# Performance work log

Hardware: AMD Instinct MI355X
Metric: run time of the kernel (lower is better)

## Reference

```python
import jax, jax.numpy as jnp
import numpy as np
from jax import lax

STRIDES = [8, 16, 32, 64, 128]
NUM_CLASSES = 80
PRE_NMS_THRESH = 0.05
PRE_NMS_TOP_N = 1000
NMS_THRESH = 0.6
MAX_DET = 100
IMG_SIZE = 800.0
BBOX_W = (10.0, 10.0, 5.0, 5.0)
SCALE_CLAMP = float(np.log(1000.0 / 16.0))  # Box2BoxTransform clamp


def conv3x3(x, w, b):
    y = lax.conv_general_dilated(x, w, (1, 1), 'SAME',
                                 dimension_numbers=('NCHW', 'OIHW', 'NCHW'))
    return y + b[None, :, None, None]


def conv1x1(x, w, b):
    return jnp.einsum('nchw,kc->nkhw', x, w) + b[None, :, None, None]


def make_anchors(H, W, stride):
    # one square anchor per location, size = 8 * stride (ATSS), offset 0.5
    size = 8.0 * stride
    xs = (jnp.arange(W, dtype=jnp.float32) + 0.5) * stride
    ys = (jnp.arange(H, dtype=jnp.float32) + 0.5) * stride
    cy, cx = jnp.meshgrid(ys, xs, indexing='ij')
    half = size / 2.0
    return jnp.stack([cx - half, cy - half, cx + half, cy + half], -1).reshape(-1, 4)


def decode(deltas, anchors):
    # Box2BoxTransform.apply_deltas with weights (10,10,5,5)
    wx, wy, ww, wh = BBOX_W
    aw = anchors[..., 2] - anchors[..., 0]
    ah = anchors[..., 3] - anchors[..., 1]
    acx = anchors[..., 0] + 0.5 * aw
    acy = anchors[..., 1] + 0.5 * ah
    dx = deltas[..., 0] / wx
    dy = deltas[..., 1] / wy
    dw = jnp.minimum(deltas[..., 2] / ww, SCALE_CLAMP)
    dh = jnp.minimum(deltas[..., 3] / wh, SCALE_CLAMP)
    pcx = dx * aw + acx
    pcy = dy * ah + acy
    pw = jnp.exp(dw) * aw
    ph = jnp.exp(dh) * ah
    boxes = jnp.stack([pcx - 0.5 * pw, pcy - 0.5 * ph,
                       pcx + 0.5 * pw, pcy + 0.5 * ph], -1)
    return jnp.clip(boxes, 0.0, IMG_SIZE)


def iou_one_vs_all(box, boxes):
    x1 = jnp.maximum(box[0], boxes[:, 0])
    y1 = jnp.maximum(box[1], boxes[:, 1])
    x2 = jnp.minimum(box[2], boxes[:, 2])
    y2 = jnp.minimum(box[3], boxes[:, 3])
    inter = jnp.clip(x2 - x1, 0.0) * jnp.clip(y2 - y1, 0.0)
    a1 = (box[2] - box[0]) * (box[3] - box[1])
    a2 = (boxes[:, 2] - boxes[:, 0]) * (boxes[:, 3] - boxes[:, 1])
    return inter / (a1 + a2 - inter + 1e-9)


def nms_single(boxes, scores, classes):
    # class-aware greedy NMS via per-class coordinate offset (ml_nms trick)
    off = classes.astype(boxes.dtype)[:, None] * (2.0 * IMG_SIZE)
    ob = boxes + off

    def step(s, _):
        i = jnp.argmax(s)
        best = s[i]
        iou = iou_one_vs_all(ob[i], ob)
        s = jnp.where(iou > NMS_THRESH, -1.0, s)
        s = s.at[i].set(-1.0)
        return s, (i, best)

    _, (idx, kept) = lax.scan(step, scores, None, length=MAX_DET)
    valid = kept > 0
    out_boxes = jnp.where(valid[:, None], boxes[idx], 0.0)
    out_scores = jnp.where(valid, kept, 0.0)
    out_classes = jnp.where(valid, classes[idx], -1)
    return out_boxes, out_scores, out_classes


def atss_forward(feats, cls_tw, cls_tb, bbox_tw, bbox_tb,
                 wcls, bcls, wbox, bbox_b, wctr, bctr, scales):
    all_boxes, all_scores, all_classes = [], [], []
    for l, x in enumerate(feats):
        c = x
        b = x
        for i in range(cls_tw.shape[0]):  # 4 tower convs
            c = jax.nn.relu(conv3x3(c, cls_tw[i], cls_tb[i]))
            b = jax.nn.relu(conv3x3(b, bbox_tw[i], bbox_tb[i]))
        logits = conv1x1(c, wcls, bcls)               # [N,C,H,W]
        deltas = scales[l] * conv1x1(b, wbox, bbox_b)  # [N,4,H,W]
        ctr = conv1x1(b, wctr, bctr)                   # [N,1,H,W]
        N, C, H, W = logits.shape
        logits = logits.transpose(0, 2, 3, 1).reshape(N, H * W, C)
        deltas = deltas.transpose(0, 2, 3, 1).reshape(N, H * W, 4)
        ctr = ctr.transpose(0, 2, 3, 1).reshape(N, H * W)
        anchors = make_anchors(H, W, STRIDES[l])       # [HW,4]
        # ATSS inference scoring: sigmoid(cls) * sigmoid(centerness)
        s = jax.nn.sigmoid(logits) * jax.nn.sigmoid(ctr)[..., None]
        s = jnp.where(s > PRE_NMS_THRESH, s, 0.0)
        flat = s.reshape(N, -1)                        # [N, HW*C]
        k = min(PRE_NMS_TOP_N, flat.shape[1])
        vals, idx = lax.top_k(flat, k)
        aidx = idx // C
        cidx = idx % C
        d = jnp.take_along_axis(deltas, aidx[:, :, None], axis=1)  # [N,k,4]
        boxes = decode(d, anchors[aidx])
        # final score = sqrt(cls*ctr); safe sqrt to avoid inf grad at 0
        sc = jnp.sqrt(jnp.where(vals > 0, vals, 1.0)) * (vals > 0)
        all_boxes.append(boxes)
        all_scores.append(sc)
        all_classes.append(cidx)
    boxes = jnp.concatenate(all_boxes, 1)
    scores = jnp.concatenate(all_scores, 1)
    classes = jnp.concatenate(all_classes, 1)
    return jax.vmap(nms_single)(boxes, scores, classes)


def setup_inputs() -> dict:
    key = jax.random.key(0)
    ks = jax.random.split(key, 12)
    feats_hw = [(100, 100), (50, 50), (25, 25), (13, 13), (7, 7)]
    N, CIN, CH = 4, 256, 256
    inp = {}
    for i, (h, w) in enumerate(feats_hw):
        inp['p%d' % (i + 3)] = jax.random.normal(ks[i], (N, CIN, h, w), jnp.float32)
    inp['cls_tw'] = jax.random.normal(ks[5], (4, CH, CIN, 3, 3), jnp.float32) * 0.02
    inp['cls_tb'] = jnp.zeros((4, CH), jnp.float32)
    inp['bbox_tw'] = jax.random.normal(ks[6], (4, CH, CIN, 3, 3), jnp.float32) * 0.02
    inp['bbox_tb'] = jnp.zeros((4, CH), jnp.float32)
    inp['wcls'] = jax.random.normal(ks[7], (NUM_CLASSES, CH), jnp.float32) * 0.05
    inp['bcls'] = jnp.zeros((NUM_CLASSES,), jnp.float32)
    inp['wbox'] = jax.random.normal(ks[8], (4, CH), jnp.float32) * 0.05
    inp['bbox_b'] = jnp.zeros((4,), jnp.float32)
    inp['wctr'] = jax.random.normal(ks[9], (1, CH), jnp.float32) * 0.05
    inp['bctr'] = jnp.zeros((1,), jnp.float32)
    inp['scales'] = jnp.ones((5,), jnp.float32)
    return inp


def reference(p3, p4, p5, p6, p7, cls_tw, cls_tb, bbox_tw, bbox_tb,
              wcls, bcls, wbox, bbox_b, wctr, bctr, scales):
    feats = [p3, p4, p5, p6, p7]
    boxes, scores, classes = atss_forward(feats, cls_tw, cls_tb, bbox_tw, bbox_tb,
                                          wcls, bcls, wbox, bbox_b, wctr, bctr, scales)
    return boxes, scores, classes
```

## Files before the change

### kernel.cpp

```cpp
#include <hip/hip_runtime.h>
#include <math.h>

typedef short s8v __attribute__((ext_vector_type(8)));
typedef short s4v __attribute__((ext_vector_type(4)));
typedef float f4v __attribute__((ext_vector_type(4)));
typedef _Float16 h8v __attribute__((ext_vector_type(8)));

__device__ __forceinline__ float sigf(float x) { return 1.f / (1.f + expf(-x)); }
__device__ __forceinline__ float f16f(short v) {
  return (float)__builtin_bit_cast(_Float16, v);
}

#define SCALE_CLAMP 4.135166556742356f
#define IMG_SIZE 800.f
#define PLANE 14482432ull
#define W_SCALE 1024.f
#define A_SCALE 64.f
#define ACC_RESCALE 1.52587890625e-5f

__device__ __forceinline__ void split2(float x, short& h, short& l) {
  _Float16 hf = (_Float16)x;
  _Float16 lf = (_Float16)(x - (float)hf);
  h = __builtin_bit_cast(short, hf);
  l = __builtin_bit_cast(short, lf);
}

struct Geo {
  int tp[6];
  int TXa[5];
  int Ha[5], Wa[5], PWa[5], PHWa[5];
  int phwOff[5];
  int hwOff[5];
  int pb[6];
  int bb[6];
};

__global__ __launch_bounds__(256) void wtrans_k(const float* __restrict__ cls_tw,
                                                const float* __restrict__ bbox_tw,
                                                short* __restrict__ wt)
{
  const int total = 589824;
  for (int u = blockIdx.x * 256 + threadIdx.x; u < total; u += gridDim.x * 256) {
    int layer = u / 73728;
    int r = u - layer * 73728;
    int tap = r / 8192;  r -= tap * 8192;
    int cc  = r / 1024;  r -= cc * 1024;
    int qq  = r / 256;   int ko = r - qq * 256;
    int cibase = cc * 32 + qq * 8;
    const float* src = (layer < 4) ? (cls_tw + (size_t)layer * 589824)
                                   : (bbox_tw + (size_t)(layer - 4) * 589824);
    s8v hv, lv;
#pragma unroll
    for (int e = 0; e < 8; ++e) {
      float x = src[(size_t)ko * 2304 + (size_t)(cibase + e) * 9 + tap] * W_SCALE;
      short h, l; split2(x, h, l);
      hv[e] = h; lv[e] = l;
    }
    size_t dbase = (size_t)layer * 1179648 + (((size_t)tap * 8 + cc) * 4 + qq) * 2048 + (size_t)ko * 8;
    *(s8v*)(wt + dbase) = hv;
    *(s8v*)(wt + dbase + 589824) = lv;
  }
}

__global__ __launch_bounds__(256) void prep_all_k(const float* __restrict__ p3, const float* __restrict__ p4,
                                                  const float* __restrict__ p5, const float* __restrict__ p6,
                                                  const float* __restrict__ p7,
                                                  short* __restrict__ out, Geo g)
{
  __shared__ float tl[64][260];
  int bx = blockIdx.x, t = threadIdx.x, n = blockIdx.y;
  int l = 0; while (l < 4 && bx >= g.pb[l + 1]) ++l;
  const float* in = (l == 0) ? p3 : (l == 1) ? p4 : (l == 2) ? p5 : (l == 3) ? p6 : p7;
  int H = g.Ha[l], W = g.Wa[l], PW = g.PWa[l], PHW = g.PHWa[l], HW = H * W;
  int P0 = (bx - g.pb[l]) * 64;
  const float* inN = in + (size_t)n * HW * 256;
  int sub = t >> 6, pl = t & 63;
  int pos = P0 + pl;
  for (int i = 0; i < 64; ++i) {
    int ci = i * 4 + sub;
    tl[pl][ci] = (pos < HW) ? inN[(size_t)ci * HW + pos] : 0.f;
  }
  __syncthreads();
  int pl2 = t >> 2, cq = (t & 3) * 64;
  int pos2 = P0 + pl2;
  if (pos2 < HW) {
    int y = pos2 / W, x = pos2 - y * W;
    size_t oo = ((size_t)g.phwOff[l] * 4 + (size_t)n * PHW + (size_t)(y + 1) * PW + (x + 1)) * 256 + cq;
#pragma unroll
    for (int grp = 0; grp < 8; ++grp) {
      s8v hv, lv;
#pragma unroll
      for (int e = 0; e < 8; ++e) {
        short h, lo; split2(tl[pl2][cq + grp * 8 + e] * A_SCALE, h, lo);
        hv[e] = h; lv[e] = lo;
      }
      *(s8v*)(out + oo + grp * 8) = hv;
      *(s8v*)(out + PLANE + oo + grp * 8) = lv;
    }
  }
}

#define QS    112
#define QVALID 108
#define PSTR  3584
#define BSTR  7168
__global__ __launch_bounds__(256, 4) void conv_all_k(const short* __restrict__ in0,
                                                     const short* __restrict__ in1,
                                                     const short* __restrict__ wt0,
                                                     const short* __restrict__ wt1,
                                                     const float* __restrict__ bias0,
                                                     const float* __restrict__ bias1,
                                                     short* __restrict__ out0,
                                                     short* __restrict__ out1, Geo g)
{
  __shared__ short act_s[2 * BSTR];

  const int t = threadIdx.x;
  const int lane = t & 63, wave = t >> 6;
  const int wcol = wave & 1, wko = wave >> 1;
  const int tower = blockIdx.z >> 2;
  const int n = blockIdx.z & 3;
  const short* in   = tower ? in1 : in0;
  const short* wtL  = tower ? wt1 : wt0;
  const float* bias = tower ? bias1 : bias0;
  short* out        = tower ? out1 : out0;
  const int ko0 = blockIdx.y * 128;
  int bx = blockIdx.x;
  int l = 0; while (l < 4 && bx >= g.tp[l + 1]) ++l;
  const int H = g.Ha[l], W = g.Wa[l], PW = g.PWa[l], PHW = g.PHWa[l];
  const int lt = bx - g.tp[l];
  const int TX = g.TXa[l];
  const int ty = lt / TX, tx = lt - ty * TX;
  const int R0 = ty * 4, C0 = tx * 16;
  const size_t bi = ((size_t)g.phwOff[l] * 4 + (size_t)n * PHW) * 256;
  const short* inN = in + bi;
  short* outN = out + bi;

  const int r = lane & 15, q = lane >> 4;
  const int cb = wcol * 8;
  const short* wlane = wtL + (size_t)q * 2048 + (size_t)(ko0 + wko * 64 + r) * 8;

  int soff[2];
#pragma unroll
  for (int k = 0; k < 2; ++k) {
    int j = t + k * 256; if (j > 447) j = 447;
    int qq = j / QS, ppos = j - qq * QS;
    int lpos = ppos - 2 * qq; if (lpos < 0) lpos += QS;
    if (lpos >= QVALID) lpos = QVALID - 1;
    int row = lpos / 18, col = lpos - row * 18;
    int prow = R0 + row; if (prow > H + 1) prow = H + 1;
    int pcol = C0 + col; if (pcol > W + 1) pcol = W + 1;
    soff[k] = (prow * PW + pcol) * 256 + qq * 8;
  }

  f4v acc[2][4];
#pragma unroll
  for (int mi = 0; mi < 2; ++mi)
#pragma unroll
    for (int ni = 0; ni < 4; ++ni) { f4v z = {0.f, 0.f, 0.f, 0.f}; acc[mi][ni] = z; }

  auto stage = [&](int cc, int buf) {
#pragma unroll
    for (int k = 0; k < 2; ++k) {
      int j = t + k * 256;
      if (j < 448) {
#pragma unroll
        for (int p = 0; p < 2; ++p) {
          const short* src = inN + (size_t)p * PLANE + (size_t)(soff[k] + cc * 32);
          short* dst = &act_s[(size_t)buf * BSTR + (size_t)p * PSTR + (size_t)j * 8];
#if __has_builtin(__builtin_amdgcn_global_load_lds)
          __builtin_amdgcn_global_load_lds((const __attribute__((address_space(1))) void*)src,
                                           (__attribute__((address_space(3))) void*)dst, 16, 0, 0);
#else
          *(s8v*)dst = *(const s8v*)src;
#endif
        }
      }
    }
  };

  auto loadW = [&](s8v (&w)[2][2], int cc2, int tap2, int half) {
    const short* base = wlane + (size_t)(tap2 * 8 + cc2) * 8192 + half * 256;
#pragma unroll
    for (int p = 0; p < 2; ++p)
#pragma unroll
      for (int k = 0; k < 2; ++k)
        w[p][k] = *(const s8v*)(base + (size_t)p * 589824 + k * 128);
  };

  auto loadA = [&](s8v (&af)[2][2], int dy, int dx, int buf) {
    const int sbase = buf * BSTR;
#pragma unroll
    for (int mi = 0; mi < 2; ++mi) {
      int lp = (2 * mi + (r >> 3) + dy) * 18 + (cb + (r & 7) + dx) + 2 * q;
      if (lp >= QS) lp -= QS;
      int sl = q * QS + lp;
      af[0][mi] = *(const s8v*)&act_s[sbase + sl * 8];
      af[1][mi] = *(const s8v*)&act_s[sbase + PSTR + sl * 8];
    }
  };

  auto runHalf = [&](const s8v (&w)[2][2], const s8v (&af)[2][2], int half) {
    const int PA[3] = {0, 0, 1};
    const int PB[3] = {0, 1, 0};
    __builtin_amdgcn_s_setprio(1);
#pragma unroll
    for (int pp = 0; pp < 3; ++pp)
#pragma unroll
      for (int mi = 0; mi < 2; ++mi)
#pragma unroll
        for (int k = 0; k < 2; ++k)
          acc[mi][half * 2 + k] = __builtin_amdgcn_mfma_f32_16x16x32_f16(
              __builtin_bit_cast(h8v, af[PA[pp]][mi]),
              __builtin_bit_cast(h8v, w[PB[pp]][k]),
              acc[mi][half * 2 + k], 0, 0, 0);
    __builtin_amdgcn_s_setprio(0);
  };

  s8v wH0[2][2], wH1[2][2], afr[2][2];
  stage(0, 0);
  loadW(wH0, 0, 0, 0);
  __syncthreads();

  int cur = 0;
  for (int cc = 0; cc < 8; ++cc) {
    if (cc < 7) stage(cc + 1, cur ^ 1);
#pragma unroll
    for (int tap = 0; tap < 9; ++tap) {
      const int dy = tap / 3, dx = tap - dy * 3;
      loadW(wH1, cc, tap, 1);
      loadA(afr, dy, dx, cur);
      runHalf(wH0, afr, 0);
      int ntap = tap + 1, ncc = cc;
      if (ntap == 9) { ntap = 0; ++ncc; }
      if (ncc < 8) loadW(wH0, ncc, ntap, 0);
      runHalf(wH1, afr, 1);
    }
    __syncthreads();
    cur ^= 1;
  }

#pragma unroll
  for (int mi = 0; mi < 2; ++mi) {
#pragma unroll
    for (int ni = 0; ni < 4; ++ni) {
      int ko = ko0 + wko * 64 + ni * 16 + r;
      float bv = bias[ko];
#pragma unroll
      for (int reg = 0; reg < 4; ++reg) {
        int rm = q * 4 + reg;
        int orow = R0 + 2 * mi + (rm >> 3);
        int ocol = C0 + cb + (rm & 7);
        if (orow < H && ocol < W) {
          float real = acc[mi][ni][reg] * ACC_RESCALE + bv;
          float vv = fmaxf(real, 0.f) * A_SCALE;
          short h, lo; split2(vv, h, lo);
          size_t oo = ((size_t)(orow + 1) * PW + (ocol + 1)) * 256 + ko;
          outN[oo] = h; outN[PLANE + oo] = lo;
        }
      }
    }
  }
}

__global__ __launch_bounds__(256) void cls_head_k(const short* __restrict__ act,
                                                  const float* __restrict__ wcls,
                                                  const float* __restrict__ bcls,
                                                  float* __restrict__ score, Geo g)
{
  __shared__ int   p2s[64];
  __shared__ float as_[64][69];
  __shared__ float ws_[64][84];
  const int t = threadIdx.x;
  const int n = blockIdx.y;
  int bx = blockIdx.x;
  int l = 0; while (l < 4 && bx >= g.pb[l + 1]) ++l;
  const int H = g.Ha[l], W = g.Wa[l], PW = g.PWa[l], PHW = g.PHWa[l], HW = H * W;
  const int P0 = (bx - g.pb[l]) * 64;
  if (t < 64) {
    int p = P0 + t; if (p >= HW) p = HW - 1;
    int y = p / W, x = p - y * W;
    p2s[t] = (y + 1) * PW + x + 1;
  }
  __syncthreads();
  float accv[4][5];
#pragma unroll
  for (int i = 0; i < 4; ++i)
#pragma unroll
    for (int j = 0; j < 5; ++j) accv[i][j] = 0.f;

  const short* actN = act + ((size_t)g.phwOff[l] * 4 + (size_t)n * PHW) * 256;
  const int pg = t >> 4, cg = t & 15;
  const float inv = 1.f / A_SCALE;

  for (int c0 = 0; c0 < 256; c0 += 64) {
    for (int i = t; i < 1024; i += 256) {
      int pos = i >> 4, c4 = i & 15;
      size_t o = (size_t)p2s[pos] * 256 + c0 + c4 * 4;
      s4v hv = *(const s4v*)(actN + o);
      s4v lv = *(const s4v*)(actN + PLANE + o);
      float* dst = &as_[pos][c4 * 4];
#pragma unroll
      for (int e = 0; e < 4; ++e) dst[e] = (f16f(hv[e]) + f16f(lv[e])) * inv;
    }
    for (int i = t; i < 1280; i += 256) {
      int c = i >> 4, c4 = i & 15;
      float4 v = *(const float4*)(wcls + (size_t)c * 256 + c0 + c4 * 4);
      ws_[c4 * 4 + 0][c] = v.x; ws_[c4 * 4 + 1][c] = v.y;
      ws_[c4 * 4 + 2][c] = v.z; ws_[c4 * 4 + 3][c] = v.w;
    }
    __syncthreads();
#pragma unroll 8
    for (int ci = 0; ci < 64; ++ci) {
#pragma unroll
      for (int i = 0; i < 4; ++i) {
        float a = as_[pg * 4 + i][ci];
#pragma unroll
        for (int j = 0; j < 5; ++j)
          accv[i][j] = fmaf(a, ws_[ci][cg * 5 + j], accv[i][j]);
      }
    }
    __syncthreads();
  }
  float* sB = score + ((size_t)g.hwOff[l] * 4 + (size_t)n * HW) * 80;
#pragma unroll
  for (int i = 0; i < 4; ++i) {
    int p = P0 + pg * 4 + i;
    if (p >= HW) continue;
#pragma unroll
    for (int j = 0; j < 5; ++j) {
      int c = cg * 5 + j;
      sB[(size_t)p * 80 + c] = sigf(accv[i][j] + bcls[c]);
    }
  }
}

__global__ __launch_bounds__(256) void box_head_k(const short* __restrict__ act,
                                                  const float* __restrict__ wbox,
                                                  const float* __restrict__ bb,
                                                  const float* __restrict__ wctr,
                                                  const float* __restrict__ bc,
                                                  const float* __restrict__ scales,
                                                  float* __restrict__ score,
                                                  float* __restrict__ deltas, Geo g)
{
  int n = blockIdx.y;
  int bx = blockIdx.x;
  int l = 0; while (l < 4 && bx >= g.bb[l + 1]) ++l;
  const int H = g.Ha[l], W = g.Wa[l], PW = g.PWa[l], PHW = g.PHWa[l], HW = H * W;
  int p = (bx - g.bb[l]) * 256 + threadIdx.x;
  if (p >= HW) return;
  int y = p / W, x = p - y * W;
  const short* a = act + ((size_t)g.phwOff[l] * 4 + (size_t)n * PHW + (size_t)(y + 1) * PW + x + 1) * 256;
  const float inv = 1.f / A_SCALE;
  float d0 = 0, d1 = 0, d2 = 0, d3 = 0, ct = 0;
  for (int gI = 0; gI < 32; ++gI) {
    s8v hv = *(const s8v*)(a + gI * 8);
    s8v lv = *(const s8v*)(a + PLANE + gI * 8);
#pragma unroll
    for (int e = 0; e < 8; ++e) {
      float av = (f16f(hv[e]) + f16f(lv[e])) * inv;
      int c = gI * 8 + e;
      d0 = fmaf(av, wbox[c], d0);
      d1 = fmaf(av, wbox[256 + c], d1);
      d2 = fmaf(av, wbox[512 + c], d2);
      d3 = fmaf(av, wbox[768 + c], d3);
      ct = fmaf(av, wctr[c], ct);
    }
  }
  float sl = scales[l];
  float* dd = deltas + ((size_t)g.hwOff[l] * 4 + (size_t)n * HW + p) * 4;
  dd[0] = sl * (d0 + bb[0]); dd[1] = sl * (d1 + bb[1]);
  dd[2] = sl * (d2 + bb[2]); dd[3] = sl * (d3 + bb[3]);
  float sct = sigf(ct + bc[0]);
  float* sp = score + ((size_t)g.hwOff[l] * 4 + (size_t)n * HW + p) * 80;
#pragma unroll
  for (int i = 0; i < 20; ++i) {
    float4 v = ((float4*)sp)[i];
    v.x *= sct; v.y *= sct; v.z *= sct; v.w *= sct;
    v.x = (v.x > 0.05f) ? v.x : 0.f;
    v.y = (v.y > 0.05f) ? v.y : 0.f;
    v.z = (v.z > 0.05f) ? v.z : 0.f;
    v.w = (v.w > 0.05f) ? v.w : 0.f;
    ((float4*)sp)[i] = v;
  }
}

__global__ __launch_bounds__(256) void hist_k(const float* __restrict__ score,
                                              const unsigned* __restrict__ thr,
                                              unsigned* __restrict__ hist, int phase, Geo g)
{
  const int grp = blockIdx.y;
  const int l = grp >> 2, n = grp & 3;
  const int HW = g.Ha[l] * g.Wa[l];
  const int M = HW * 80;
  const float* s = score + ((size_t)g.hwOff[l] * 4 + (size_t)n * HW) * 80;
  unsigned* h = hist + grp * 2048;
  const unsigned* tr = thr + grp * 8;
  __shared__ unsigned lh[2048];
  for (int i = threadIdx.x; i < 2048; i += 256) lh[i] = 0u;
  __syncthreads();
  unsigned B1 = 0, pref = 0;
  if (phase == 1) B1 = tr[0];
  if (phase == 2) pref = (tr[0] << 11) | tr[1];
  for (int idx = blockIdx.x * 256 + threadIdx.x; idx < M; idx += gridDim.x * 256) {
    float v = s[idx];
    if (v > 0.f) {
      unsigned b = __float_as_uint(v);
      if (phase == 0) atomicAdd(&lh[b >> 20], 1u);
      else if (phase == 1) { if ((b >> 20) == B1) atomicAdd(&lh[(b >> 9) & 0x7FFu], 1u); }
      else { if ((b >> 9) == pref) atomicAdd(&lh[b & 0x1FFu], 1u); }
    }
  }
  __syncthreads();
  for (int i = threadIdx.x; i < 2048; i += 256) { unsigned v = lh[i]; if (v) atomicAdd(&h[i], v); }
}

__global__ __launch_bounds__(256) void scan_k(unsigned* __restrict__ hist,
                                              unsigned* __restrict__ thr, int phase)
{
  const int grp = blockIdx.x, t = threadIdx.x;
  unsigned* h  = hist + grp * 2048;
  unsigned* tr = thr + grp * 8;
  const int nb = (phase == 2) ? 512 : 2048;
  const int PB = nb / 256;
  unsigned target = 1000u;
  bool dead = false;
  if (phase >= 1) {
    target = 1000u - tr[2];
    if (tr[0] == 0xFFFFFFFFu) dead = true;
    if (phase == 2 && tr[1] == 0xFFFFFFFFu) dead = true;
  }
  __shared__ unsigned ps[256];
  __shared__ unsigned s_tot;
  const int hi = nb - t * PB;
  unsigned lsum = 0;
  for (int k = 0; k < PB; ++k) lsum += h[hi - 1 - k];
  ps[t] = lsum;
  __syncthreads();
  if (t == 0) {
    unsigned cum = 0;
    for (int i = 0; i < 256; ++i) { unsigned tmp = ps[i]; ps[i] = cum; cum += tmp; }
    s_tot = cum;
  }
  __syncthreads();
  unsigned exc = ps[t], tot = s_tot;
  if (!dead && tot >= target) {
    if (exc < target && exc + lsum >= target) {
      unsigned cum = exc; int bf = 0; unsigned above = 0;
      for (int k = 0; k < PB; ++k) {
        int bidx = hi - 1 - k;
        unsigned c = h[bidx];
        if (cum < target && cum + c >= target) { bf = bidx; above = cum; }
        cum += c;
      }
      if (phase == 0)      { tr[0] = (unsigned)bf; tr[2] = above; }
      else if (phase == 1) { tr[1] = (unsigned)bf; tr[2] = tr[2] + above; }
      else {
        unsigned T = (tr[0] << 20) | (tr[1] << 9) | (unsigned)bf;
        tr[3] = T; tr[4] = target - above;
      }
    }
  } else if (t == 0) {
    if (phase == 0)      { tr[0] = 0xFFFFFFFFu; tr[2] = 0u; }
    else if (phase == 1) { tr[1] = 0xFFFFFFFFu; }
    else                 { tr[3] = 0u; tr[4] = 0u; }
  }
  if (phase == 2 && t == 0) { tr[5] = 0u; tr[6] = 0u; }
}

__global__ __launch_bounds__(256) void select_k(const float* __restrict__ score,
                                                const float* __restrict__ deltas,
                                                unsigned* __restrict__ thr,
                                                float* __restrict__ cbox, float* __restrict__ csc,
                                                float* __restrict__ ccls, float* __restrict__ cgid,
                                                Geo g)
{
  const int grp = blockIdx.y;
  const int l = grp >> 2, n = grp & 3;
  const int W = g.Wa[l];
  const int HW = g.Ha[l] * W;
  const int M = HW * 80;
  const float stride_ = (float)(8 << l);
  const float* s = score + ((size_t)g.hwOff[l] * 4 + (size_t)n * HW) * 80;
  const float* dBase = deltas + ((size_t)g.hwOff[l] * 4 + (size_t)n * HW) * 4;
  unsigned* tr = thr + grp * 8;
  const unsigned T = tr[3], need = tr[4];
  for (int idx = blockIdx.x * 256 + threadIdx.x; idx < M; idx += gridDim.x * 256) {
    float v = s[idx];
    if (!(v > 0.f)) continue;
    unsigned b = __float_as_uint(v);
    int slot = -1;
    if (b > T) slot = (int)atomicAdd(&tr[5], 1u);
    else if (b == T) {
      unsigned e = atomicAdd(&tr[6], 1u);
      if (e < need) slot = (int)(1000u - need + e);
    }
    if (slot < 0) continue;
    int p = idx / 80, c = idx - p * 80;
    int y = p / W, x = p - y * W;
    const float* d = dBase + (size_t)p * 4;
    float sz  = 8.f * stride_;
    float acx = ((float)x + 0.5f) * stride_;
    float acy = ((float)y + 0.5f) * stride_;
    float dx = d[0] / 10.f, dy = d[1] / 10.f;
    float dw = fminf(d[2] / 5.f, SCALE_CLAMP);
    float dh = fminf(d[3] / 5.f, SCALE_CLAMP);
    float pcx = dx * sz + acx;
    float pcy = dy * sz + acy;
    float pw = expf(dw) * sz;
    float ph = expf(dh) * sz;
    float x1 = pcx - 0.5f * pw, y1_ = pcy - 0.5f * ph;
    float x2 = pcx + 0.5f * pw, y2_ = pcy + 0.5f * ph;
    x1  = fminf(fmaxf(x1, 0.f),  IMG_SIZE);
    y1_ = fminf(fmaxf(y1_, 0.f), IMG_SIZE);
    x2  = fminf(fmaxf(x2, 0.f),  IMG_SIZE);
    y2_ = fminf(fmaxf(y2_, 0.f), IMG_SIZE);
    int cslot = n * 5000 + l * 1000 + slot;
    ((float4*)cbox)[cslot] = make_float4(x1, y1_, x2, y2_);
    csc[cslot]  = sqrtf(v);
    ccls[cslot] = (float)c;
    cgid[cslot] = (float)(((unsigned)l << 20) | (unsigned)idx);
  }
}

__global__ __launch_bounds__(256) void nms_k(const float* __restrict__ cbox,
                                             const float* __restrict__ csc,
                                             const float* __restrict__ ccls,
                                             const float* __restrict__ cgid,
                                             float* __restrict__ outp)
{
  const int n = blockIdx.x, t = threadIdx.x;
  float sc[20], cl[20], gid[20], bx[20][4];
#pragma unroll
  for (int j = 0; j < 20; ++j) {
    int gidx = j * 256 + t;
    if (gidx < 5000) {
      sc[j] = csc[n * 5000 + gidx];
      float4 b = ((const float4*)cbox)[n * 5000 + gidx];
      bx[j][0] = b.x; bx[j][1] = b.y; bx[j][2] = b.z; bx[j][3] = b.w;
      cl[j]  = ccls[n * 5000 + gidx];
      gid[j] = cgid[n * 5000 + gidx];
    } else { sc[j] = -2.f; bx[j][0] = bx[j][1] = bx[j][2] = bx[j][3] = 0.f; cl[j] = 0.f; gid[j] = 1e9f; }
  }
  __shared__ float rv[4]; __shared__ int rg[4]; __shared__ float rgid[4];
  __shared__ float sbox[4]; __shared__ float scls; __shared__ float sval; __shared__ int sgi;

  for (int it = 0; it < 100; ++it) {
    float bv = -3.f; int bg = 0; float bgid = 2e9f;
#pragma unroll
    for (int j = 0; j < 20; ++j) {
      bool better = (sc[j] > bv) || (sc[j] == bv && gid[j] < bgid);
      if (better) { bv = sc[j]; bg = j * 256 + t; bgid = gid[j]; }
    }
    for (int off = 32; off; off >>= 1) {
      float ov = __shfl_xor(bv, off);
      int   og = __shfl_xor(bg, off);
      float oi = __shfl_xor(bgid, off);
      bool better = (ov > bv) || (ov == bv && oi < bgid);
      if (better) { bv = ov; bg = og; bgid = oi; }
    }
    int wid = t >> 6;
    if ((t & 63) == 0) { rv[wid] = bv; rg[wid] = bg; rgid[wid] = bgid; }
    __syncthreads();
    if (t == 0) {
      float fv = rv[0]; int fg = rg[0]; float fi = rgid[0];
      for (int w = 1; w < 4; ++w) {
        bool better = (rv[w] > fv) || (rv[w] == fv && rgid[w] < fi);
        if (better) { fv = rv[w]; fg = rg[w]; fi = rgid[w]; }
      }
      sval = fv; sgi = fg;
    }
    __syncthreads();
    float best_v = sval; int best_g = sgi;
    if (t == (best_g & 255)) {
      int j = best_g >> 8;
      sbox[0] = bx[j][0]; sbox[1] = bx[j][1]; sbox[2] = bx[j][2]; sbox[3] = bx[j][3];
      scls = cl[j];
    }
    __syncthreads();
    bool valid = best_v > 0.f;
    if (t == 0) {
      int base = n * 100 + it;
      outp[base * 4 + 0] = valid ? sbox[0] : 0.f;
      outp[base * 4 + 1] = valid ? sbox[1] : 0.f;
      outp[base * 4 + 2] = valid ? sbox[2] : 0.f;
      outp[base * 4 + 3] = valid ? sbox[3] : 0.f;
      outp[1600 + base] = valid ? best_v : 0.f;
      outp[2000 + base] = valid ? scls : -1.f;
    }
    float off_ = scls * (2.f * IMG_SIZE);
    float e0 = sbox[0] + off_, e1 = sbox[1] + off_, e2 = sbox[2] + off_, e3 = sbox[3] + off_;
    float a1 = (e2 - e0) * (e3 - e1);
#pragma unroll
    for (int j = 0; j < 20; ++j) {
      float o_ = cl[j] * (2.f * IMG_SIZE);
      float f0 = bx[j][0] + o_, f1 = bx[j][1] + o_, f2 = bx[j][2] + o_, f3 = bx[j][3] + o_;
      float xx1 = fmaxf(e0, f0), yy1 = fmaxf(e1, f1);
      float xx2 = fminf(e2, f2), yy2 = fminf(e3, f3);
      float inter = fmaxf(xx2 - xx1, 0.f) * fmaxf(yy2 - yy1, 0.f);
      float a2 = (f2 - f0) * (f3 - f1);
      float iou = inter / (a1 + a2 - inter + 1e-9f);
      if (iou > 0.6f) sc[j] = -1.f;
      if ((j * 256 + t) == best_g) sc[j] = -1.f;
    }
    __syncthreads();
  }
}

extern "C" void kernel_launch(void* const* d_in, const int* in_sizes, int n_in,
                              void* d_out, int out_size, void* d_ws, size_t ws_size,
                              hipStream_t stream)
{
  (void)in_sizes; (void)n_in; (void)out_size; (void)ws_size;
  const float* p3 = (const float*)d_in[0];
  const float* p4 = (const float*)d_in[1];
  const float* p5 = (const float*)d_in[2];
  const float* p6 = (const float*)d_in[3];
  const float* p7 = (const float*)d_in[4];
  const float* cls_tw  = (const float*)d_in[5];
  const float* cls_tb  = (const float*)d_in[6];
  const float* bbox_tw = (const float*)d_in[7];
  const float* bbox_tb = (const float*)d_in[8];
  const float* wcls    = (const float*)d_in[9];
  const float* bcls    = (const float*)d_in[10];
  const float* wbox    = (const float*)d_in[11];
  const float* bbox_b  = (const float*)d_in[12];
  const float* wctr    = (const float*)d_in[13];
  const float* bctr    = (const float*)d_in[14];
  const float* scales  = (const float*)d_in[15];
  float* out = (float*)d_out;

  Geo G;
  const int Hs[5] = {100, 50, 25, 13, 7};
  {
    int tpre = 0, ppre = 0, bpre = 0, phw = 0, hw = 0;
    for (int l = 0; l < 5; ++l) {
      int H = Hs[l], W = Hs[l];
      G.Ha[l] = H; G.Wa[l] = W; G.PWa[l] = W + 2; G.PHWa[l] = (H + 2) * (W + 2);
      G.TXa[l] = (W + 15) / 16;
      int TY = (H + 3) / 4;
      G.tp[l] = tpre;  tpre += G.TXa[l] * TY;
      G.pb[l] = ppre;  ppre += (H * W + 63) / 64;
      G.bb[l] = bpre;  bpre += (H * W + 255) / 256;
      G.phwOff[l] = phw; phw += G.PHWa[l];
      G.hwOff[l]  = hw;  hw  += H * W;
    }
    G.tp[5] = tpre; G.pb[5] = ppre; G.bb[5] = bpre;
  }
  const int nTiles = G.tp[5];
  const int nPrep  = G.pb[5];
  const int nBoxB  = G.bb[5];
  const int sumHW = 13343;
  const size_t scoreBytes  = (size_t)sumHW * 4 * 80 * 4;
  const size_t deltasBytes = (size_t)sumHW * 4 * 4 * 4;

  char* ws = (char*)d_ws;
  size_t off = 0;
  auto alloc = [&](size_t bytes) -> void* {
    off = (off + 255) & ~(size_t)255;
    void* p = ws + off; off += bytes; return p;
  };
  const size_t bufBytes = 2ull * PLANE * 2;

  short* wt     = (short*)alloc((size_t)8 * 2 * 589824 * 2);
  float* cbox   = (float*)alloc(4ull * 5000 * 4 * 4);
  float* csc    = (float*)alloc(4ull * 5000 * 4);
  float* ccls   = (float*)alloc(4ull * 5000 * 4);
  float* cgid   = (float*)alloc(4ull * 5000 * 4);
  unsigned* hist = (unsigned*)alloc(20ull * 2048 * 4);
  unsigned* thr  = (unsigned*)alloc(20ull * 8 * 4);
  short* A = (short*)alloc(bufBytes);
  short* B = (short*)alloc(bufBytes);
  float* score  = (float*)alloc(scoreBytes);
  float* deltas = (float*)alloc(deltasBytes);

  hipMemsetAsync(cbox, 0, 4ull * 5000 * 4 * 4, stream);
  hipMemsetAsync(csc,  0, 4ull * 5000 * 4, stream);
  hipMemsetAsync(ccls, 0, 4ull * 5000 * 4, stream);
  hipMemsetAsync(cgid, 0, 4ull * 5000 * 4, stream);
  hipMemsetAsync(thr,  0, 20ull * 8 * 4, stream);
  hipMemsetAsync(A, 0, bufBytes, stream);
  hipMemsetAsync(B, 0, bufBytes, stream);

  wtrans_k<<<1024, 256, 0, stream>>>(cls_tw, bbox_tw, wt);

  const size_t LSTRIDE = 2ull * 589824;
  dim3 cg(nTiles, 2, 4);

  prep_all_k<<<dim3(nPrep, 4), 256, 0, stream>>>(p3, p4, p5, p6, p7, A, G);
  conv_all_k<<<cg, 256, 0, stream>>>(A, A, wt + 0 * LSTRIDE, wt + 0 * LSTRIDE,
                                     cls_tb + 0 * 256, cls_tb + 0 * 256, B, B, G);
  conv_all_k<<<cg, 256, 0, stream>>>(B, B, wt + 1 * LSTRIDE, wt + 1 * LSTRIDE,
                                     cls_tb + 1 * 256, cls_tb + 1 * 256, A, A, G);
  conv_all_k<<<cg, 256, 0, stream>>>(A, A, wt + 2 * LSTRIDE, wt + 2 * LSTRIDE,
                                     cls_tb + 2 * 256, cls_tb + 2 * 256, B, B, G);
  conv_all_k<<<cg, 256, 0, stream>>>(B, B, wt + 3 * LSTRIDE, wt + 3 * LSTRIDE,
                                     cls_tb + 3 * 256, cls_tb + 3 * 256, A, A, G);
  cls_head_k<<<dim3(nPrep, 4), 256, 0, stream>>>(A, wcls, bcls, score, G);
  prep_all_k<<<dim3(nPrep, 4), 256, 0, stream>>>(p3, p4, p5, p6, p7, B, G);
  conv_all_k<<<cg, 256, 0, stream>>>(B, B, wt + 4 * LSTRIDE, wt + 4 * LSTRIDE,
                                     bbox_tb + 0 * 256, bbox_tb + 0 * 256, A, A, G);
  conv_all_k<<<cg, 256, 0, stream>>>(A, A, wt + 5 * LSTRIDE, wt + 5 * LSTRIDE,
                                     bbox_tb + 1 * 256, bbox_tb + 1 * 256, B, B, G);
  conv_all_k<<<cg, 256, 0, stream>>>(B, B, wt + 6 * LSTRIDE, wt + 6 * LSTRIDE,
                                     bbox_tb + 2 * 256, bbox_tb + 2 * 256, A, A, G);
  conv_all_k<<<cg, 256, 0, stream>>>(A, A, wt + 7 * LSTRIDE, wt + 7 * LSTRIDE,
                                     bbox_tb + 3 * 256, bbox_tb + 3 * 256, B, B, G);
  box_head_k<<<dim3(nBoxB, 4), 256, 0, stream>>>(B, wbox, bbox_b, wctr, bctr, scales,
                                                 score, deltas, G);

  const int hb = 196;
  for (int phase = 0; phase < 3; ++phase) {
    hipMemsetAsync(hist, 0, 20ull * 2048 * 4, stream);
    hist_k<<<dim3(hb, 20), 256, 0, stream>>>(score, thr, hist, phase, G);
    scan_k<<<20, 256, 0, stream>>>(hist, thr, phase);
  }
  select_k<<<dim3(hb, 20), 256, 0, stream>>>(score, deltas, thr, cbox, csc, ccls, cgid, G);

  nms_k<<<4, 256, 0, stream>>>(cbox, csc, ccls, cgid, out);
}
```

Before: 2.223 ms.

## Split NMS into per-class bucketed NMS blocks plus top-k merge

Replaces the single-block-per-image greedy NMS with three kernels. The first buckets candidates by class with packed score/id keys, the second runs independent per-class NMS in parallel blocks, and the third merges the per-class kept lists into the top 100. This exploits the fact that class-aware NMS only suppresses within a class, which removes the long serial 100-iteration loop over all 5000 candidates per image. The cost is two extra kernel launches and workspace buffers. The bucketing also uses shared-memory atomics, so ties may be ordered differently.

```diff
diff --git a/kernel.cpp b/kernel.cpp
--- a/kernel.cpp
+++ b/kernel.cpp
@@ -524,85 +524,140 @@
   }
 }
 
-__global__ __launch_bounds__(256) void nms_k(const float* __restrict__ cbox,
-                                             const float* __restrict__ csc,
-                                             const float* __restrict__ ccls,
-                                             const float* __restrict__ cgid,
-                                             float* __restrict__ outp)
-{
+__global__ __launch_bounds__(256) void nms_bucket_k(const float* __restrict__ cbox,
+                                                    const float* __restrict__ csc,
+                                                    const float* __restrict__ ccls,
+                                                    const float* __restrict__ cgid,
+                                                    float4* __restrict__ bbox2,
+                                                    unsigned long long* __restrict__ bkey2,
+                                                    int* __restrict__ coff)
+{
+  __shared__ unsigned cnt[80];
+  __shared__ unsigned off_s[81];
   const int n = blockIdx.x, t = threadIdx.x;
-  float sc[20], cl[20], gid[20], bx[20][4];
-#pragma unroll
-  for (int j = 0; j < 20; ++j) {
-    int gidx = j * 256 + t;
-    if (gidx < 5000) {
-      sc[j] = csc[n * 5000 + gidx];
-      float4 b = ((const float4*)cbox)[n * 5000 + gidx];
-      bx[j][0] = b.x; bx[j][1] = b.y; bx[j][2] = b.z; bx[j][3] = b.w;
-      cl[j]  = ccls[n * 5000 + gidx];
-      gid[j] = cgid[n * 5000 + gidx];
-    } else { sc[j] = -2.f; bx[j][0] = bx[j][1] = bx[j][2] = bx[j][3] = 0.f; cl[j] = 0.f; gid[j] = 1e9f; }
-  }
-  __shared__ float rv[4]; __shared__ int rg[4]; __shared__ float rgid[4];
-  __shared__ float sbox[4]; __shared__ float scls; __shared__ float sval; __shared__ int sgi;
-
+  for (int i = t; i < 80; i += 256) cnt[i] = 0u;
+  __syncthreads();
+  for (int i = t; i < 5000; i += 256) {
+    float s = csc[n * 5000 + i];
+    if (s > 0.f) atomicAdd(&cnt[(int)ccls[n * 5000 + i]], 1u);
+  }
+  __syncthreads();
+  if (t == 0) {
+    unsigned c = 0;
+    for (int k = 0; k < 80; ++k) { off_s[k] = c; c += cnt[k]; }
+    off_s[80] = c;
+  }
+  __syncthreads();
+  for (int i = t; i < 81; i += 256) coff[n * 81 + i] = (int)off_s[i];
+  for (int i = t; i < 80; i += 256) cnt[i] = 0u;
+  __syncthreads();
+  for (int i = t; i < 5000; i += 256) {
+    float s = csc[n * 5000 + i];
+    if (s > 0.f) {
+      int c = (int)ccls[n * 5000 + i];
+      unsigned p = atomicAdd(&cnt[c], 1u);
+      int dst = n * 5000 + (int)off_s[c] + (int)p;
+      bbox2[dst] = ((const float4*)cbox)[n * 5000 + i];
+      unsigned long long sb = (unsigned long long)__float_as_uint(s);
+      unsigned gid = (unsigned)cgid[n * 5000 + i];
+      bkey2[dst] = (sb << 24) | (unsigned long long)(0xFFFFFFu - gid);
+    }
+  }
+}
+
+__global__ __launch_bounds__(64) void nms_class_k(const float4* __restrict__ bbox2,
+                                                  const unsigned long long* __restrict__ bkey2,
+                                                  const int* __restrict__ coff,
+                                                  float4* __restrict__ kbox,
+                                                  unsigned long long* __restrict__ kkey,
+                                                  int* __restrict__ kcnt)
+{
+  __shared__ unsigned long long key_s[5000];
+  const int cls = blockIdx.x, n = blockIdx.y, t = threadIdx.x;
+  const int lo = coff[n * 81 + cls], hi = coff[n * 81 + cls + 1];
+  const int c = hi - lo;
+  const int base = n * 5000 + lo;
+  for (int i = t; i < c; i += 64) key_s[i] = bkey2[base + i];
+  __syncthreads();
+  const int outB = (n * 80 + cls) * 100;
+  int kept = 0;
+  while (kept < 100) {
+    unsigned long long best = 0ull; int bi = 0;
+    for (int i = t; i < c; i += 64) {
+      unsigned long long k = key_s[i];
+      if (k > best) { best = k; bi = i; }
+    }
+#pragma unroll
+    for (int o = 32; o; o >>= 1) {
+      unsigned long long ok = __shfl_xor(best, o);
+      int oi = __shfl_xor(bi, o);
+      if (ok > best) { best = ok; bi = oi; }
+    }
+    if (best == 0ull) break;
+    float4 wb = bbox2[base + bi];
+    if (t == 0) {
+      kbox[outB + kept] = wb;
+      kkey[outB + kept] = best;
+      key_s[bi] = 0ull;
+    }
+    ++kept;
+    float a1 = (wb.z - wb.x) * (wb.w - wb.y);
+    for (int i = t; i < c; i += 64) {
+      if (key_s[i] == 0ull) continue;
+      float4 b = bbox2[base + i];
+      float xx1 = fmaxf(wb.x, b.x), yy1 = fmaxf(wb.y, b.y);
+      float xx2 = fminf(wb.z, b.z), yy2 = fminf(wb.w, b.w);
+      float inter = fmaxf(xx2 - xx1, 0.f) * fmaxf(yy2 - yy1, 0.f);
+      float a2 = (b.z - b.x) * (b.w - b.y);
+      float iou = inter / (a1 + a2 - inter + 1e-9f);
+      if (iou > 0.6f) key_s[i] = 0ull;
+    }
+    __syncthreads();
+  }
+  if (t == 0) kcnt[n * 80 + cls] = kept;
+}
+
+__global__ __launch_bounds__(64) void nms_merge_k(const float4* __restrict__ kbox,
+                                                  const unsigned long long* __restrict__ kkey,
+                                                  const int* __restrict__ kcnt,
+                                                  float* __restrict__ outp)
+{
+  __shared__ int head[80];
+  __shared__ int cnts[80];
+  const int n = blockIdx.x, t = threadIdx.x;
+  for (int i = t; i < 80; i += 64) { head[i] = 0; cnts[i] = kcnt[n * 80 + i]; }
+  __syncthreads();
   for (int it = 0; it < 100; ++it) {
-    float bv = -3.f; int bg = 0; float bgid = 2e9f;
-#pragma unroll
-    for (int j = 0; j < 20; ++j) {
-      bool better = (sc[j] > bv) || (sc[j] == bv && gid[j] < bgid);
-      if (better) { bv = sc[j]; bg = j * 256 + t; bgid = gid[j]; }
-    }
-    for (int off = 32; off; off >>= 1) {
-      float ov = __shfl_xor(bv, off);
-      int   og = __shfl_xor(bg, off);
-      float oi = __shfl_xor(bgid, off);
-      bool better = (ov > bv) || (ov == bv && oi < bgid);
-      if (better) { bv = ov; bg = og; bgid = oi; }
-    }
-    int wid = t >> 6;
-    if ((t & 63) == 0) { rv[wid] = bv; rg[wid] = bg; rgid[wid] = bgid; }
-    __syncthreads();
+    unsigned long long best = 0ull; int bc = 0;
+    for (int cls = t; cls < 80; cls += 64) {
+      int h = head[cls];
+      if (h < cnts[cls]) {
+        unsigned long long k = kkey[(n * 80 + cls) * 100 + h];
+        if (k > best) { best = k; bc = cls; }
+      }
+    }
+#pragma unroll
+    for (int o = 32; o; o >>= 1) {
+      unsigned long long ok = __shfl_xor(best, o);
+      int oc = __shfl_xor(bc, o);
+      if (ok > best) { best = ok; bc = oc; }
+    }
     if (t == 0) {
-      float fv = rv[0]; int fg = rg[0]; float fi = rgid[0];
-      for (int w = 1; w < 4; ++w) {
-        bool better = (rv[w] > fv) || (rv[w] == fv && rgid[w] < fi);
-        if (better) { fv = rv[w]; fg = rg[w]; fi = rgid[w]; }
+      int basei = n * 100 + it;
+      if (best != 0ull) {
+        int idx = (n * 80 + bc) * 100 + head[bc];
+        float4 b = kbox[idx];
+        outp[basei * 4 + 0] = b.x; outp[basei * 4 + 1] = b.y;
+        outp[basei * 4 + 2] = b.z; outp[basei * 4 + 3] = b.w;
+        outp[1600 + basei] = __uint_as_float((unsigned)(best >> 24));
+        outp[2000 + basei] = (float)bc;
+        head[bc] = head[bc] + 1;
+      } else {
+        outp[basei * 4 + 0] = 0.f; outp[basei * 4 + 1] = 0.f;
+        outp[basei * 4 + 2] = 0.f; outp[basei * 4 + 3] = 0.f;
+        outp[1600 + basei] = 0.f;
+        outp[2000 + basei] = -1.f;
       }
-      sval = fv; sgi = fg;
-    }
-    __syncthreads();
-    float best_v = sval; int best_g = sgi;
-    if (t == (best_g & 255)) {
-      int j = best_g >> 8;
-      sbox[0] = bx[j][0]; sbox[1] = bx[j][1]; sbox[2] = bx[j][2]; sbox[3] = bx[j][3];
-      scls = cl[j];
-    }
-    __syncthreads();
-    bool valid = best_v > 0.f;
-    if (t == 0) {
-      int base = n * 100 + it;
-      outp[base * 4 + 0] = valid ? sbox[0] : 0.f;
-      outp[base * 4 + 1] = valid ? sbox[1] : 0.f;
-      outp[base * 4 + 2] = valid ? sbox[2] : 0.f;
-      outp[base * 4 + 3] = valid ? sbox[3] : 0.f;
-      outp[1600 + base] = valid ? best_v : 0.f;
-      outp[2000 + base] = valid ? scls : -1.f;
-    }
-    float off_ = scls * (2.f * IMG_SIZE);
-    float e0 = sbox[0] + off_, e1 = sbox[1] + off_, e2 = sbox[2] + off_, e3 = sbox[3] + off_;
-    float a1 = (e2 - e0) * (e3 - e1);
-#pragma unroll
-    for (int j = 0; j < 20; ++j) {
-      float o_ = cl[j] * (2.f * IMG_SIZE);
-      float f0 = bx[j][0] + o_, f1 = bx[j][1] + o_, f2 = bx[j][2] + o_, f3 = bx[j][3] + o_;
-      float xx1 = fmaxf(e0, f0), yy1 = fmaxf(e1, f1);
-      float xx2 = fminf(e2, f2), yy2 = fminf(e3, f3);
-      float inter = fmaxf(xx2 - xx1, 0.f) * fmaxf(yy2 - yy1, 0.f);
-      float a2 = (f2 - f0) * (f3 - f1);
-      float iou = inter / (a1 + a2 - inter + 1e-9f);
-      if (iou > 0.6f) sc[j] = -1.f;
-      if ((j * 256 + t) == best_g) sc[j] = -1.f;
     }
     __syncthreads();
   }
@@ -670,12 +725,17 @@
   float* cgid   = (float*)alloc(4ull * 5000 * 4);
   unsigned* hist = (unsigned*)alloc(20ull * 2048 * 4);
   unsigned* thr  = (unsigned*)alloc(20ull * 8 * 4);
+  float4* bbox2 = (float4*)alloc(4ull * 5000 * 16);
+  unsigned long long* bkey2 = (unsigned long long*)alloc(4ull * 5000 * 8);
+  int* coff     = (int*)alloc(4ull * 81 * 4);
+  float4* kbox  = (float4*)alloc(320ull * 100 * 16);
+  unsigned long long* kkey = (unsigned long long*)alloc(320ull * 100 * 8);
+  int* kcnt     = (int*)alloc(320ull * 4);
   short* A = (short*)alloc(bufBytes);
   short* B = (short*)alloc(bufBytes);
   float* score  = (float*)alloc(scoreBytes);
   float* deltas = (float*)alloc(deltasBytes);
 
-  hipMemsetAsync(cbox, 0, 4ull * 5000 * 4 * 4, stream);
   hipMemsetAsync(csc,  0, 4ull * 5000 * 4, stream);
   hipMemsetAsync(ccls, 0, 4ull * 5000 * 4, stream);
   hipMemsetAsync(cgid, 0, 4ull * 5000 * 4, stream);
@@ -718,5 +778,7 @@
   }
   select_k<<<dim3(hb, 20), 256, 0, stream>>>(score, deltas, thr, cbox, csc, ccls, cgid, G);
 
-  nms_k<<<4, 256, 0, stream>>>(cbox, csc, ccls, cgid, out);
-}
+  nms_bucket_k<<<4, 256, 0, stream>>>(cbox, csc, ccls, cgid, bbox2, bkey2, coff);
+  nms_class_k<<<dim3(80, 4), 64, 0, stream>>>(bbox2, bkey2, coff, kbox, kkey, kcnt);
+  nms_merge_k<<<4, 64, 0, stream>>>(kbox, kkey, kcnt, out);
+}
```

Result: slower. 2.269 ms (+2.1%).
